# Kernel optimization log

Hardware: AMD Instinct MI355X
Metric: run time of the kernel (lower is better)

## Reference

```python
import jax, jax.numpy as jnp
import numpy as np

NUM_HEADS = 64
DIM = 128
# Rotation schedule: all (i, j) with i < j in row-major order, matching
# GivensRotationPerHead._create_rotation_indices. R = DIM*(DIM-1)//2 = 8128.
_II, _JJ = np.triu_indices(DIM, k=1)


def setup_inputs() -> dict:
    key = jax.random.key(0)
    thetas = jax.random.normal(key, (NUM_HEADS, _II.shape[0]), dtype=jnp.float32) * 0.01
    return {
        "thetas": thetas,
        "rot_i": jnp.asarray(_II, dtype=jnp.int32),
        "rot_j": jnp.asarray(_JJ, dtype=jnp.int32),
    }


def reference(thetas, rot_i, rot_j):
    # thetas: [H, R]; rot_i, rot_j: [R]
    H, R = thetas.shape
    dim = DIM
    # Precompute all cos/sin once ([R, H, 1]) instead of per-step trig.
    c = jnp.cos(thetas.T)[:, :, None]
    s = jnp.sin(thetas.T)[:, :, None]
    Q0 = jnp.broadcast_to(jnp.eye(dim, dtype=thetas.dtype), (H, dim, dim))

    def body(Q, xs):
        i, j, ci, si = xs
        Qi = Q[:, i, :]  # [H, dim]
        Qj = Q[:, j, :]  # [H, dim]
        Q = Q.at[:, i, :].set(ci * Qi + si * Qj)
        Q = Q.at[:, j, :].set(-si * Qi + ci * Qj)
        return Q, None

    Q, _ = jax.lax.scan(body, Q0, (rot_i, rot_j, c, s))
    return Q
```

## Files before the change

kernel.cpp:

```cpp
#include <hip/hip_runtime.h>

#define DIM 128
#define NHEAD 64
#define NROT 8128
#define NSEG7 7
#define MHEAD7 25600
#define KAC 168
#define CSROWS 64

typedef float f4 __attribute__((ext_vector_type(4)));
typedef short bf8 __attribute__((ext_vector_type(8)));
typedef unsigned short u16;

__device__ const int C_A0[NSEG7]   = {0,0,0,32,32,64,96};
__device__ const int C_J0[NSEG7]   = {32,64,96,64,96,96,128};
__device__ const int C_NJ[NSEG7]   = {32,32,32,32,32,32,0};
__device__ const int C_N[NSEG7]    = {64,64,64,64,64,64,32};
__device__ const int C_OFF[NSEG7]  = {0,4096,8192,12288,16384,20480,24576};
__device__ const int C_INTRA[NSEG7]= {1,0,0,1,0,1,1};

__device__ __forceinline__ void sincos_poly(float x, float& sn, float& cn) {
    float x2 = x * x;
    sn = x * fmaf(x2, fmaf(x2, 8.33333333e-3f, -1.66666667e-1f), 1.0f);
    cn = fmaf(x2, fmaf(x2, 4.16666667e-2f, -0.5f), 1.0f);
}

__device__ __forceinline__ u16 f2bf(float v) {
    unsigned b = __float_as_uint(v);
    b += 0x7FFF + ((b >> 16) & 1);
    return (u16)(b >> 16);
}
__device__ __forceinline__ float bf2f(u16 h) {
    return __uint_as_float(((unsigned)h) << 16);
}

__device__ __forceinline__ int tri_base(int i) {
    return (i * (2 * DIM - 1 - i)) >> 1;
}

__device__ __forceinline__ void store_bf(u16* oh, u16* ol, int idx, float v, bool act) {
    u16 h = f2bf(v);
    u16 l = f2bf(v - bf2f(h));
    if (act) { oh[idx] = h; ol[idx] = l; }
}

__global__ __launch_bounds__(64, 1)
void chain7(const float* __restrict__ th_all,
            u16* __restrict__ MhW, u16* __restrict__ MlW)
{
    __shared__ __align__(16) float csx[992 + 32 * 64];

    const int lane = threadIdx.x;
    const int head = blockIdx.x & 63;
    const int s    = blockIdx.x >> 6;
    const int a0 = C_A0[s], j0 = C_J0[s], nj = C_NJ[s], n = C_N[s];
    const bool intra = C_INTRA[s] != 0;
    const float* __restrict__ th = th_all + head * NROT;
    u16* __restrict__ oh = MhW + (size_t)head * MHEAD7 + C_OFF[s];
    u16* __restrict__ ol = MlW + (size_t)head * MHEAD7 + C_OFF[s];
    const bool cact = lane < n;
    const int ne = 32 * nj;
    const int d1 = j0 - a0 - 1;

    float thx[16];
    #pragma unroll
    for (int it = 0; it < 16; ++it) {
        if (it * 64 < ne) {
            int e = lane + it * 64;
            int t = e & 31, r = e >> 5;
            thx[it] = th[tri_base(a0 + t) + d1 + r - t];
        }
    }
    float thi[8];
    #pragma unroll
    for (int it = 0; it < 8; ++it) {
        int e = lane + it * 64;
        if (intra && e < 496) {
            int t1 = 0, rem = e;
            while (rem >= 31 - t1) { rem -= 31 - t1; ++t1; }
            int t2 = t1 + 1 + rem;
            thi[it] = th[tri_base(a0 + t1) + (t2 - t1 - 1)];
        }
    }
    #pragma unroll
    for (int it = 0; it < 16; ++it) {
        if (it * 64 < ne) {
            int e = lane + it * 64;
            float sn, cn; sincos_poly(thx[it], sn, cn);
            csx[992 + 2 * e] = cn; csx[992 + 2 * e + 1] = sn;
        }
    }
    #pragma unroll
    for (int it = 0; it < 8; ++it) {
        int e = lane + it * 64;
        if (intra && e < 496) {
            float sn, cn; sincos_poly(thi[it], sn, cn);
            csx[2 * e] = cn; csx[2 * e + 1] = sn;
        }
    }
    __syncthreads();

    float p[32];
    #pragma unroll
    for (int t = 0; t < 32; ++t) p[t] = (lane == t) ? 1.0f : 0.0f;

    if (intra) {
        f4 cc;
        int idx = 0;
        #pragma unroll
        for (int t1 = 0; t1 < 31; ++t1) {
            #pragma unroll
            for (int t2 = t1 + 1; t2 < 32; ++t2) {
                float c, sn;
                if ((idx & 1) == 0) { cc = *(const f4*)&csx[2 * idx]; c = cc.x; sn = cc.y; }
                else                { c = cc.z; sn = cc.w; }
                float pa = p[t1];
                p[t1] = fmaf(c, pa,    sn * p[t2]);
                p[t2] = fmaf(c, p[t2], -(sn * pa));
                ++idx;
            }
        }
    }

    if (nj > 0) {
        const float* cs = csx + 992;
        const int jv = lane - 32;
        #pragma unroll 2
        for (int r = 0; r < nj; ++r) {
            const f4* c4 = (const f4*)(cs + r * 64);
            f4 q[16];
            #pragma unroll
            for (int i = 0; i < 16; ++i) q[i] = c4[i];
            float v = (r == jv) ? 1.0f : 0.0f;
            #pragma unroll
            for (int t = 0; t < 32; t += 2) {
                f4 qq = q[t >> 1];
                { float pv = p[t];     float nv = fmaf(qq.x, v, -(qq.y * pv));
                  p[t]     = fmaf(qq.y, v, qq.x * pv); v = nv; }
                { float pv = p[t + 1]; float nv = fmaf(qq.z, v, -(qq.w * pv));
                  p[t + 1] = fmaf(qq.w, v, qq.z * pv); v = nv; }
            }
            store_bf(oh, ol, (32 + r) * n + lane, v, cact);
        }
    }

    #pragma unroll
    for (int t = 0; t < 32; ++t)
        store_bf(oh, ol, t * n + lane, p[t], cact);
}

__global__ __launch_bounds__(256, 1)
void compose7(const u16* __restrict__ MhA, const u16* __restrict__ MlA,
              float* __restrict__ out)
{
    __shared__ u16 AhT[16][KAC];
    __shared__ u16 AlT[16][KAC];

    const int tid  = threadIdx.x;
    const int lane = tid & 63;
    const int w    = tid >> 6;
    const int head = blockIdx.x & 63;
    const int sl   = blockIdx.x >> 6;
    const int c0   = sl * 16;
    const u16* __restrict__ Mh = MhA + (size_t)head * MHEAD7;
    const u16* __restrict__ Ml = MlA + (size_t)head * MHEAD7;

    {
        int c = tid & 15, rr = tid >> 4, cg = c0 + c;
        for (int k = DIM + rr; k < KAC; k += 16) { AhT[c][k] = 0; AlT[c][k] = 0; }
        for (int r = rr; r < DIM; r += 16) {
            u16 h, l;
            if (r < 64 && cg < 64) { h = Mh[r * 64 + cg]; l = Ml[r * 64 + cg]; }
            else                   { h = (r == cg) ? (u16)0x3F80 : (u16)0; l = 0; }
            AhT[c][r] = h; AlT[c][r] = l;
        }
    }
    __syncthreads();

    const int fr = lane & 15;
    const int fk = (lane >> 4) * 8;
    const int r4 = (lane >> 4) * 4;
    const int ro = 16 * w;

    auto ldM = [&](int s, bf8& ah0, bf8& al0, bf8& ah1, bf8& al1) {
        const int n = C_N[s];
        const u16* __restrict__ Msh = Mh + C_OFF[s];
        const u16* __restrict__ Msl = Ml + C_OFF[s];
        const int rA  = ro + fr;
        const int rAc = (rA < n) ? rA : (n - 1);
        const int kx  = 32 + fk;
        const int kc1 = (kx <= n - 8) ? kx : (n - 8);
        ah0 = *(const bf8*)&Msh[(size_t)rAc * n + fk];
        al0 = *(const bf8*)&Msl[(size_t)rAc * n + fk];
        ah1 = *(const bf8*)&Msh[(size_t)rAc * n + kc1];
        al1 = *(const bf8*)&Msl[(size_t)rAc * n + kc1];
    };

    bf8 cah0, cal0, cah1, cal1, nah0, nal0, nah1, nal1;
    ldM(1, cah0, cal0, cah1, cal1);

    #pragma unroll 1
    for (int s = 1; s < NSEG7; ++s) {
        const int a0 = C_A0[s], j0 = C_J0[s], n = C_N[s];

        const int kx = 32 + fk;
        const int b0 = a0 + fk;
        const int b1 = (kx < n) ? (j0 + fk) : 128;
        bf8 bh0 = *(const bf8*)&AhT[fr][b0];
        bf8 bl0 = *(const bf8*)&AlT[fr][b0];
        bf8 bh1 = *(const bf8*)&AhT[fr][b1];
        bf8 bl1 = *(const bf8*)&AlT[fr][b1];

        if (s + 1 < NSEG7) ldM(s + 1, nah0, nal0, nah1, nal1);

        const bool act = ro < n;
        f4 acc = {0, 0, 0, 0};
        if (act) {
            acc = __builtin_amdgcn_mfma_f32_16x16x32_bf16(cah0, bh0, acc, 0, 0, 0);
            acc = __builtin_amdgcn_mfma_f32_16x16x32_bf16(cah0, bl0, acc, 0, 0, 0);
            acc = __builtin_amdgcn_mfma_f32_16x16x32_bf16(cal0, bh0, acc, 0, 0, 0);
            acc = __builtin_amdgcn_mfma_f32_16x16x32_bf16(cal0, bl0, acc, 0, 0, 0);
            acc = __builtin_amdgcn_mfma_f32_16x16x32_bf16(cah1, bh1, acc, 0, 0, 0);
            acc = __builtin_amdgcn_mfma_f32_16x16x32_bf16(cah1, bl1, acc, 0, 0, 0);
            acc = __builtin_amdgcn_mfma_f32_16x16x32_bf16(cal1, bh1, acc, 0, 0, 0);
            acc = __builtin_amdgcn_mfma_f32_16x16x32_bf16(cal1, bl1, acc, 0, 0, 0);
        }

        __syncthreads();

        const int rowq = ro + r4;
        if (act && rowq < n) {
            const int rg = (rowq < 32) ? (a0 + rowq) : (j0 + rowq - 32);
            float v0 = acc[0], v1 = acc[1], v2 = acc[2], v3 = acc[3];
            u16 h0 = f2bf(v0), h1 = f2bf(v1), h2 = f2bf(v2), h3 = f2bf(v3);
            u16 l0 = f2bf(v0 - bf2f(h0)), l1 = f2bf(v1 - bf2f(h1));
            u16 l2 = f2bf(v2 - bf2f(h2)), l3 = f2bf(v3 - bf2f(h3));
            ushort4 hv; hv.x = h0; hv.y = h1; hv.z = h2; hv.w = h3;
            ushort4 lv; lv.x = l0; lv.y = l1; lv.z = l2; lv.w = l3;
            *(ushort4*)&AhT[fr][rg] = hv;
            *(ushort4*)&AlT[fr][rg] = lv;
        }
        __syncthreads();

        cah0 = nah0; cal0 = nal0; cah1 = nah1; cal1 = nal1;
    }

    {
        int c = tid & 15, rr = tid >> 4;
        float* o = out + (size_t)head * (DIM * DIM) + c0;
        for (int r = rr; r < DIM; r += 16)
            o[r * DIM + c] = bf2f(AhT[c][r]) + bf2f(AlT[c][r]);
    }
}

struct Row8 { f4 q0, q1, q2, q3; };
__device__ __forceinline__ void ldrow_u(Row8& R, const float* p) {
    const f4* c4 = (const f4*)p;
    R.q0 = c4[0]; R.q1 = c4[1]; R.q2 = c4[2]; R.q3 = c4[3];
}
#define QA(r, c) Q[(r)][ (c) ^ ((r) & 31) ]
#define ROTP(c, s, T, v) { float pt = p[T]; p[T] = fmaf((c), pt, (s) * (v)); \
                           (v) = fmaf((c), (v), -((s) * pt)); }
__device__ __forceinline__ void rot8q(const Row8& r, float p[8], float& v) {
    ROTP(r.q0.x, r.q0.y, 0, v) ROTP(r.q0.z, r.q0.w, 1, v)
    ROTP(r.q1.x, r.q1.y, 2, v) ROTP(r.q1.z, r.q1.w, 3, v)
    ROTP(r.q2.x, r.q2.y, 4, v) ROTP(r.q2.z, r.q2.w, 5, v)
    ROTP(r.q3.x, r.q3.y, 6, v) ROTP(r.q3.z, r.q3.w, 7, v)
}

__global__ __launch_bounds__(64, 1)
void chain_mono(const float* __restrict__ th_all, float* __restrict__ outp)
{
    __shared__ float Q[DIM][64];
    __shared__ __align__(16) float csx[56 + CSROWS * 16];

    const int lane = threadIdx.x;
    const int head = blockIdx.x & 63;
    const int cb   = blockIdx.x >> 6;
    const int col_glob = cb * 64 + lane;
    const float* __restrict__ th = th_all + head * NROT;

    for (int r = 0; r < DIM; ++r)
        QA(r, lane) = (r == col_glob) ? 1.0f : 0.0f;

    #pragma unroll 1
    for (int g = 0; g < 16; ++g) {
        const int a0  = 8 * g;
        const int ntr = 120 - a0;
        float p[8];
        const int nsub = (ntr > CSROWS) ? 2 : 1;
        #pragma unroll 1
        for (int sub = 0; sub < nsub; ++sub) {
            const int r0 = sub * CSROWS;
            const int nr = (ntr - r0) < CSROWS ? (ntr - r0) : CSROWS;
            const int ne = 8 * nr;
            __syncthreads();
            float thx[8];
            #pragma unroll
            for (int it = 0; it < 8; ++it) {
                if (it * 64 < ne) {
                    int e = lane + it * 64;
                    int t = e & 7, jr = r0 + (e >> 3);
                    thx[it] = th[tri_base(a0 + t) + jr + 7 - t];
                }
            }
            float thi = 0.0f;
            if (sub == 0 && lane < 28) {
                int t1 = 0, rem = lane;
                while (rem >= 7 - t1) { rem -= 7 - t1; ++t1; }
                int t2 = t1 + 1 + rem;
                thi = th[tri_base(a0 + t1) + (t2 - t1 - 1)];
            }
            #pragma unroll
            for (int it = 0; it < 8; ++it) {
                if (it * 64 < ne) {
                    int e = lane + it * 64;
                    float sn, cn; sincos_poly(thx[it], sn, cn);
                    csx[56 + 2 * e] = cn; csx[56 + 2 * e + 1] = sn;
                }
            }
            if (sub == 0 && lane < 28) {
                float sn, cn; sincos_poly(thi, sn, cn);
                csx[2 * lane] = cn; csx[2 * lane + 1] = sn;
            }
            __syncthreads();

            if (sub == 0) {
                #pragma unroll
                for (int t = 0; t < 8; ++t) p[t] = QA(a0 + t, lane);
                int idx = 0;
                #pragma unroll
                for (int t1 = 0; t1 < 8; ++t1) {
                    #pragma unroll
                    for (int t2 = t1 + 1; t2 < 8; ++t2) {
                        float c = csx[2 * idx], sn = csx[2 * idx + 1];
                        float pa = p[t1];
                        p[t1] = fmaf(c, pa,    sn * p[t2]);
                        p[t2] = fmaf(c, p[t2], -(sn * pa));
                        ++idx;
                    }
                }
            }
            if (nr > 0) {
                const float* cs = csx + 56;
                const int base = a0 + 8 + r0;
                Row8 A0, A1, B0, B1;
                float vA0, vA1, vB0, vB1;
                auto ldpair = [&](Row8& R, float& v, int r) {
                    ldrow_u(R, cs + 16 * r);
                    v = QA(base + r, lane);
                };
                ldpair(A0, vA0, 0); ldpair(A1, vA1, 1);
                #pragma unroll 1
                for (int r = 0; r < nr; r += 4) {
                    ldpair(B0, vB0, r + 2); ldpair(B1, vB1, r + 3);
                    rot8q(A0, p, vA0); rot8q(A1, p, vA1);
                    QA(base + r, lane)     = vA0;
                    QA(base + r + 1, lane) = vA1;
                    if (r + 4 < nr) { ldpair(A0, vA0, r + 4); ldpair(A1, vA1, r + 5); }
                    rot8q(B0, p, vB0); rot8q(B1, p, vB1);
                    QA(base + r + 2, lane) = vB0;
                    QA(base + r + 3, lane) = vB1;
                }
            }
        }
        #pragma unroll
        for (int t = 0; t < 8; ++t) QA(a0 + t, lane) = p[t];
    }

    __syncthreads();
    float* o = outp + head * (DIM * DIM) + col_glob;
    #pragma unroll 1
    for (int r = 0; r < DIM; ++r) o[r * DIM] = QA(r, lane);
}

extern "C" void kernel_launch(void* const* d_in, const int* in_sizes, int n_in,
                              void* d_out, int out_size, void* d_ws, size_t ws_size,
                              hipStream_t stream) {
    const float* thetas = (const float*)d_in[0];
    float* out = (float*)d_out;
    const size_t need = (size_t)NHEAD * MHEAD7 * 2 * sizeof(u16);

    if (ws_size >= need) {
        u16* MhW = (u16*)d_ws;
        u16* MlW = MhW + (size_t)NHEAD * MHEAD7;
        chain7<<<dim3(NSEG7 * NHEAD), dim3(64), 0, stream>>>(thetas, MhW, MlW);
        compose7<<<dim3(8 * NHEAD), dim3(256), 0, stream>>>(MhW, MlW, out);
    } else {
        chain_mono<<<dim3(2 * NHEAD), dim3(64), 0, stream>>>(thetas, out);
    }
}
```

Measured before the change: 39.87 us.

## Stage all segment matrices in swizzled LDS and widen compose blocks to 32 columns

The compose kernel now bulk-copies every per-head segment matrix (hi and lo bf16 parts) into shared memory with an XOR swizzle before the segment loop. MFMA A-operands are then read from LDS instead of from global memory on each step. Each block also covers 32 output columns with 8 waves instead of 16 columns with 4 waves, which halves the grid and the redundant per-head matrix reads. The cost is roughly 100KB of shared memory per block, which limits occupancy to one block per CU, plus an up-front load phase that is not overlapped with compute.

```diff
diff --git a/kernel.cpp b/kernel.cpp
--- a/kernel.cpp
+++ b/kernel.cpp
@@ -3,28 +3,28 @@
 #define DIM 128
 #define NHEAD 64
 #define NROT 8128
-#define NSEG7 7
+#define NSEG 7
 #define MHEAD7 25600
-#define KAC 168
+#define KAC 136
 #define CSROWS 64
 
 typedef float f4 __attribute__((ext_vector_type(4)));
 typedef short bf8 __attribute__((ext_vector_type(8)));
 typedef unsigned short u16;
 
-__device__ const int C_A0[NSEG7]   = {0,0,0,32,32,64,96};
-__device__ const int C_J0[NSEG7]   = {32,64,96,64,96,96,128};
-__device__ const int C_NJ[NSEG7]   = {32,32,32,32,32,32,0};
-__device__ const int C_N[NSEG7]    = {64,64,64,64,64,64,32};
-__device__ const int C_OFF[NSEG7]  = {0,4096,8192,12288,16384,20480,24576};
-__device__ const int C_INTRA[NSEG7]= {1,0,0,1,0,1,1};
+__device__ const int C_A0[NSEG]    = {0,0,0,32,32,64,96};
+__device__ const int C_J0[NSEG]    = {32,64,96,64,96,96,128};
+__device__ const int C_NJ[NSEG]    = {32,32,32,32,32,32,0};
+__device__ const int C_N[NSEG]     = {64,64,64,64,64,64,32};
+__device__ const int C_OFF[NSEG]   = {0,4096,8192,12288,16384,20480,24576};
+__device__ const int C_INTRA[NSEG] = {1,0,0,1,0,1,1};
+__device__ const int C_LB[NSEG]    = {0,8192,16384,24576,32768,40960,49152};
 
 __device__ __forceinline__ void sincos_poly(float x, float& sn, float& cn) {
     float x2 = x * x;
     sn = x * fmaf(x2, fmaf(x2, 8.33333333e-3f, -1.66666667e-1f), 1.0f);
     cn = fmaf(x2, fmaf(x2, 4.16666667e-2f, -0.5f), 1.0f);
 }
-
 __device__ __forceinline__ u16 f2bf(float v) {
     unsigned b = __float_as_uint(v);
     b += 0x7FFF + ((b >> 16) & 1);
@@ -33,11 +33,7 @@
 __device__ __forceinline__ float bf2f(u16 h) {
     return __uint_as_float(((unsigned)h) << 16);
 }
-
-__device__ __forceinline__ int tri_base(int i) {
-    return (i * (2 * DIM - 1 - i)) >> 1;
-}
-
+__device__ __forceinline__ int tri_base(int i) { return (i * (2 * DIM - 1 - i)) >> 1; }
 __device__ __forceinline__ void store_bf(u16* oh, u16* ol, int idx, float v, bool act) {
     u16 h = f2bf(v);
     u16 l = f2bf(v - bf2f(h));
@@ -78,8 +74,7 @@
         if (intra && e < 496) {
             int t1 = 0, rem = e;
             while (rem >= 31 - t1) { rem -= 31 - t1; ++t1; }
-            int t2 = t1 + 1 + rem;
-            thi[it] = th[tri_base(a0 + t1) + (t2 - t1 - 1)];
+            thi[it] = th[tri_base(a0 + t1) + rem];
         }
     }
     #pragma unroll
@@ -105,8 +100,7 @@
     for (int t = 0; t < 32; ++t) p[t] = (lane == t) ? 1.0f : 0.0f;
 
     if (intra) {
-        f4 cc;
-        int idx = 0;
+        f4 cc; int idx = 0;
         #pragma unroll
         for (int t1 = 0; t1 < 31; ++t1) {
             #pragma unroll
@@ -149,107 +143,124 @@
         store_bf(oh, ol, t * n + lane, p[t], cact);
 }
 
-__global__ __launch_bounds__(256, 1)
-void compose7(const u16* __restrict__ MhA, const u16* __restrict__ MlA,
-              float* __restrict__ out)
+__global__ __launch_bounds__(512, 1)
+void compose_lds(const u16* __restrict__ MhA, const u16* __restrict__ MlA,
+                 float* __restrict__ out)
 {
-    __shared__ u16 AhT[16][KAC];
-    __shared__ u16 AlT[16][KAC];
+    __shared__ u16 Msw[51200];
+    __shared__ u16 Ah[32][KAC];
+    __shared__ u16 Al[32][KAC];
 
     const int tid  = threadIdx.x;
     const int lane = tid & 63;
     const int w    = tid >> 6;
     const int head = blockIdx.x & 63;
-    const int sl   = blockIdx.x >> 6;
-    const int c0   = sl * 16;
+    const int q    = blockIdx.x >> 6;
     const u16* __restrict__ Mh = MhA + (size_t)head * MHEAD7;
     const u16* __restrict__ Ml = MlA + (size_t)head * MHEAD7;
 
-    {
-        int c = tid & 15, rr = tid >> 4, cg = c0 + c;
-        for (int k = DIM + rr; k < KAC; k += 16) { AhT[c][k] = 0; AlT[c][k] = 0; }
-        for (int r = rr; r < DIM; r += 16) {
-            u16 h, l;
-            if (r < 64 && cg < 64) { h = Mh[r * 64 + cg]; l = Ml[r * 64 + cg]; }
-            else                   { h = (r == cg) ? (u16)0x3F80 : (u16)0; l = 0; }
-            AhT[c][r] = h; AlT[c][r] = l;
-        }
+    #pragma unroll 1
+    for (int s = 0; s < NSEG; ++s) {
+        const int n = C_N[s];
+        const int lsh = (n == 32) ? 2 : 3;
+        const int msk = (1 << lsh) - 1;
+        const int nch = (n * n) >> 3;
+        const u16* gh = Mh + C_OFF[s];
+        const u16* gl = Ml + C_OFF[s];
+        u16* lb = Msw + C_LB[s];
+        const int nn = n * n;
+        for (int ch = tid; ch < nch; ch += 512) {
+            int r  = ch >> lsh;
+            int kb = ch & msk;
+            int dst = r * n + (((kb ^ (r & msk)) & msk) << 3);
+            *(uint4*)&lb[dst]      = *(const uint4*)&gh[ch << 3];
+            *(uint4*)&lb[nn + dst] = *(const uint4*)&gl[ch << 3];
+        }
+    }
+    __syncthreads();
+
+    for (int i = tid; i < 32 * KAC; i += 512) {
+        int c = i / KAC, k = i - c * KAC;
+        int cg = q * 32 + c;
+        u16 h = 0, l = 0;
+        if (k < 64) {
+            if (cg < 64) {
+                int idx = k * 64 + ((((cg >> 3) ^ (k & 7)) & 7) << 3) + (cg & 7);
+                h = Msw[idx]; l = Msw[4096 + idx];
+            }
+        } else if (k < 128) {
+            h = (k == cg) ? (u16)0x3F80 : (u16)0;
+        }
+        Ah[c][k] = h; Al[c][k] = l;
     }
     __syncthreads();
 
     const int fr = lane & 15;
     const int fk = (lane >> 4) * 8;
     const int r4 = (lane >> 4) * 4;
-    const int ro = 16 * w;
-
-    auto ldM = [&](int s, bf8& ah0, bf8& al0, bf8& ah1, bf8& al1) {
-        const int n = C_N[s];
-        const u16* __restrict__ Msh = Mh + C_OFF[s];
-        const u16* __restrict__ Msl = Ml + C_OFF[s];
-        const int rA  = ro + fr;
-        const int rAc = (rA < n) ? rA : (n - 1);
-        const int kx  = 32 + fk;
-        const int kc1 = (kx <= n - 8) ? kx : (n - 8);
-        ah0 = *(const bf8*)&Msh[(size_t)rAc * n + fk];
-        al0 = *(const bf8*)&Msl[(size_t)rAc * n + fk];
-        ah1 = *(const bf8*)&Msh[(size_t)rAc * n + kc1];
-        al1 = *(const bf8*)&Msl[(size_t)rAc * n + kc1];
-    };
-
-    bf8 cah0, cal0, cah1, cal1, nah0, nal0, nah1, nal1;
-    ldM(1, cah0, cal0, cah1, cal1);
 
     #pragma unroll 1
-    for (int s = 1; s < NSEG7; ++s) {
-        const int a0 = C_A0[s], j0 = C_J0[s], n = C_N[s];
-
-        const int kx = 32 + fk;
-        const int b0 = a0 + fk;
-        const int b1 = (kx < n) ? (j0 + fk) : 128;
-        bf8 bh0 = *(const bf8*)&AhT[fr][b0];
-        bf8 bl0 = *(const bf8*)&AlT[fr][b0];
-        bf8 bh1 = *(const bf8*)&AhT[fr][b1];
-        bf8 bl1 = *(const bf8*)&AlT[fr][b1];
-
-        if (s + 1 < NSEG7) ldM(s + 1, nah0, nal0, nah1, nal1);
-
-        const bool act = ro < n;
+    for (int s = 1; s < NSEG; ++s) {
+        const int a0 = C_A0[s], j0 = C_J0[s], n = C_N[s], LB = C_LB[s];
+        const int lsh = (n == 32) ? 2 : 3;
+        const int gmsk = (1 << lsh) - 1;
+        const int nn = n * n;
+        const int nrt = n >> 4;
+        const bool act = w < nrt * 2;
+        const int rt = w >> 1, ct = w & 1;
+
         f4 acc = {0, 0, 0, 0};
         if (act) {
-            acc = __builtin_amdgcn_mfma_f32_16x16x32_bf16(cah0, bh0, acc, 0, 0, 0);
-            acc = __builtin_amdgcn_mfma_f32_16x16x32_bf16(cah0, bl0, acc, 0, 0, 0);
-            acc = __builtin_amdgcn_mfma_f32_16x16x32_bf16(cal0, bh0, acc, 0, 0, 0);
-            acc = __builtin_amdgcn_mfma_f32_16x16x32_bf16(cal0, bl0, acc, 0, 0, 0);
-            acc = __builtin_amdgcn_mfma_f32_16x16x32_bf16(cah1, bh1, acc, 0, 0, 0);
-            acc = __builtin_amdgcn_mfma_f32_16x16x32_bf16(cah1, bl1, acc, 0, 0, 0);
-            acc = __builtin_amdgcn_mfma_f32_16x16x32_bf16(cal1, bh1, acc, 0, 0, 0);
-            acc = __builtin_amdgcn_mfma_f32_16x16x32_bf16(cal1, bl1, acc, 0, 0, 0);
-        }
-
+            const int rA = rt * 16 + fr;
+            const int c  = ct * 16 + fr;
+            auto mload = [&](int kc, bf8& mh, bf8& ml) {
+                int idx = LB + rA * n + ((((kc >> 3) ^ (rA & gmsk)) & gmsk) << 3);
+                mh = *(const bf8*)&Msw[idx];
+                ml = *(const bf8*)&Msw[idx + nn];
+            };
+            bf8 mh0, ml0;
+            mload(fk, mh0, ml0);
+            bf8 bh0 = *(const bf8*)&Ah[c][a0 + fk];
+            bf8 bl0 = *(const bf8*)&Al[c][a0 + fk];
+            acc = __builtin_amdgcn_mfma_f32_16x16x32_bf16(mh0, bh0, acc, 0, 0, 0);
+            acc = __builtin_amdgcn_mfma_f32_16x16x32_bf16(mh0, bl0, acc, 0, 0, 0);
+            acc = __builtin_amdgcn_mfma_f32_16x16x32_bf16(ml0, bh0, acc, 0, 0, 0);
+            acc = __builtin_amdgcn_mfma_f32_16x16x32_bf16(ml0, bl0, acc, 0, 0, 0);
+            if (n == 64) {
+                bf8 mh1, ml1;
+                mload(32 + fk, mh1, ml1);
+                bf8 bh1 = *(const bf8*)&Ah[c][j0 + fk];
+                bf8 bl1 = *(const bf8*)&Al[c][j0 + fk];
+                acc = __builtin_amdgcn_mfma_f32_16x16x32_bf16(mh1, bh1, acc, 0, 0, 0);
+                acc = __builtin_amdgcn_mfma_f32_16x16x32_bf16(mh1, bl1, acc, 0, 0, 0);
+                acc = __builtin_amdgcn_mfma_f32_16x16x32_bf16(ml1, bh1, acc, 0, 0, 0);
+                acc = __builtin_amdgcn_mfma_f32_16x16x32_bf16(ml1, bl1, acc, 0, 0, 0);
+            }
+        }
         __syncthreads();
 
-        const int rowq = ro + r4;
-        if (act && rowq < n) {
+        if (act) {
+            const int rowq = rt * 16 + r4;
             const int rg = (rowq < 32) ? (a0 + rowq) : (j0 + rowq - 32);
+            const int c  = ct * 16 + fr;
             float v0 = acc[0], v1 = acc[1], v2 = acc[2], v3 = acc[3];
             u16 h0 = f2bf(v0), h1 = f2bf(v1), h2 = f2bf(v2), h3 = f2bf(v3);
             u16 l0 = f2bf(v0 - bf2f(h0)), l1 = f2bf(v1 - bf2f(h1));
             u16 l2 = f2bf(v2 - bf2f(h2)), l3 = f2bf(v3 - bf2f(h3));
             ushort4 hv; hv.x = h0; hv.y = h1; hv.z = h2; hv.w = h3;
             ushort4 lv; lv.x = l0; lv.y = l1; lv.z = l2; lv.w = l3;
-            *(ushort4*)&AhT[fr][rg] = hv;
-            *(ushort4*)&AlT[fr][rg] = lv;
+            *(ushort4*)&Ah[c][rg] = hv;
+            *(ushort4*)&Al[c][rg] = lv;
         }
         __syncthreads();
-
-        cah0 = nah0; cal0 = nal0; cah1 = nah1; cal1 = nal1;
     }
 
     {
-        int c = tid & 15, rr = tid >> 4;
-        float* o = out + (size_t)head * (DIM * DIM) + c0;
-        for (int r = rr; r < DIM; r += 16)
-            o[r * DIM + c] = bf2f(AhT[c][r]) + bf2f(AlT[c][r]);
+        float* o = out + (size_t)head * (DIM * DIM) + q * 32;
+        for (int i = tid; i < 32 * DIM; i += 512) {
+            int c = i & 31, r = i >> 5;
+            o[r * DIM + c] = bf2f(Ah[c][r]) + bf2f(Al[c][r]);
+        }
     }
 }
 
@@ -384,8 +395,8 @@
     if (ws_size >= need) {
         u16* MhW = (u16*)d_ws;
         u16* MlW = MhW + (size_t)NHEAD * MHEAD7;
-        chain7<<<dim3(NSEG7 * NHEAD), dim3(64), 0, stream>>>(thetas, MhW, MlW);
-        compose7<<<dim3(8 * NHEAD), dim3(256), 0, stream>>>(MhW, MlW, out);
+        chain7<<<dim3(NSEG * NHEAD), dim3(64), 0, stream>>>(thetas, MhW, MlW);
+        compose_lds<<<dim3(4 * NHEAD), dim3(512), 0, stream>>>(MhW, MlW, out);
     } else {
         chain_mono<<<dim3(2 * NHEAD), dim3(64), 0, stream>>>(thetas, out);
     }
```

Result: no change. 39.65 us (-0.6%).
